# Performance work log

Measured on AMD Instinct MI355X. Metric: run time of the kernel, lower is better.

Reference implementation:

```python
import jax, jax.numpy as jnp
import numpy as np

WIN = (2, 6, 12)          # (vert, lat, lon) window size
HEADS = 6
DIM = 192
TYPES = 64                # type_of_windows = ceil(8/2)*ceil(96/6)
N = WIN[0] * WIN[1] * WIN[2]   # 144 patches per window


def _position_index():
    wz, wh, ww = WIN
    zi = np.arange(wz); zj = -np.arange(wz) * wz
    hi = np.arange(wh); hj = -np.arange(wh) * wh
    w = np.arange(ww)
    c1 = np.stack(np.meshgrid(zi, hi, w, indexing='ij')).reshape(3, -1)
    c2 = np.stack(np.meshgrid(zj, hj, w, indexing='ij')).reshape(3, -1)
    coords = (c1[:, :, None] - c2[:, None, :]).transpose(1, 2, 0)  # (N, N, 3)
    coords[:, :, 2] += ww - 1
    coords[:, :, 1] *= 2 * ww - 1
    coords[:, :, 0] *= (2 * ww - 1) * wh * wh
    return coords.sum(-1).reshape(-1)  # (N*N,) int

POS_IDX = jnp.asarray(_position_index())


def setup_inputs() -> dict:
    key = jax.random.key(0)
    ks = jax.random.split(key, 7)
    B = 960   # n_batch(1) * type_of_windows(64) * lon_windows(15)
    return {
        "x": jax.random.normal(ks[0], (B, N, DIM), jnp.float32),
        "mask": jax.random.normal(ks[1], (15, N, N), jnp.float32),
        "w_qkv": jax.random.normal(ks[2], (DIM, 3 * DIM), jnp.float32) * 0.02,
        "b_qkv": jax.random.normal(ks[3], (3 * DIM,), jnp.float32) * 0.02,
        "w_out": jax.random.normal(ks[4], (DIM, DIM), jnp.float32) * 0.02,
        "b_out": jax.random.normal(ks[5], (DIM,), jnp.float32) * 0.02,
        "bias_table": jax.random.normal(ks[6], (3312, TYPES, HEADS), jnp.float32) * 0.02,
    }


def reference(x, mask, w_qkv, b_qkv, w_out, b_out, bias_table):
    B = x.shape[0]
    hd = DIM // HEADS
    scale = hd ** -0.5

    qkv = (x @ w_qkv + b_qkv).reshape(B, N, 3, HEADS, hd)
    q, k, v = jnp.transpose(qkv, (2, 0, 3, 1, 4))      # each (B, H, N, hd)

    attn = jnp.einsum('bhnd,bhmd->bhnm', q * scale, k)  # (B, H, N, N)

    # gathered earth-specific absolute position bias: (TYPES, H, N, N)
    bias = bias_table[POS_IDX].reshape(N, N, TYPES, HEADS).transpose(2, 3, 0, 1)
    attn = (attn.reshape(-1, TYPES, HEADS, N, N) + bias[None]).reshape(B, HEADS, N, N)

    # additive mask over longitude-shifted windows
    n_w = mask.shape[0]
    attn = attn.reshape(B // n_w, n_w, HEADS, N, N) + mask[None, :, None]
    attn = attn.reshape(B, HEADS, N, N)

    attn = jax.nn.softmax(attn, axis=-1)               # dropout = identity (eval)

    out = jnp.einsum('bhnm,bhmd->bhnd', attn, v)       # (B, H, N, hd)
    out = out.transpose(0, 2, 1, 3).reshape(B, N, DIM)
    return out @ w_out + b_out
```

## Files before the change

### kernel.cpp

```cpp
#include <hip/hip_runtime.h>
#include <stdint.h>

typedef __bf16 bf16;
typedef __bf16 bf16x4 __attribute__((ext_vector_type(4)));
typedef __bf16 bf16x8 __attribute__((ext_vector_type(8)));
typedef float  f32x4  __attribute__((ext_vector_type(4)));

#define MFMA16(A, B, C) __builtin_amdgcn_mfma_f32_16x16x32_bf16((A), (B), (C), 0, 0, 0)

#define LOG2E 1.4426950408889634f


__global__ __launch_bounds__(256) void k_prep(const float* __restrict__ wqkv,
                                              const float* __restrict__ wout,
                                              bf16* __restrict__ wqkvt,
                                              bf16* __restrict__ woutt) {
    int i = blockIdx.x * 256 + threadIdx.x;
    if (i < 576 * 192) {
        int blk = i >> 9;
        int within = i & 511;
        int lane = within >> 3, j = within & 7;
        int strip = blk / 6, ks = blk - strip * 6;
        int col = strip * 16 + (lane & 15);
        int k = ks * 32 + (lane >> 4) * 8 + j;
        wqkvt[i] = (bf16)wqkv[k * 576 + col];
    } else {
        int jj = i - 576 * 192;
        int blk = jj >> 9;
        int within = jj & 511;
        int lane = within >> 3, j = within & 7;
        int strip = blk / 6, ks = blk - strip * 6;
        int col = strip * 16 + (lane & 15);
        int k = ks * 32 + (lane >> 4) * 8 + j;
        woutt[jj] = (bf16)wout[k * 192 + col];
    }
}

__global__ __launch_bounds__(256) void k_bias(const float* __restrict__ btab,
                                              bf16* __restrict__ bias) {
    __shared__ float tb[3312];
    const int th = blockIdx.x;
    for (int i = threadIdx.x; i < 3312; i += 256)
        tb[i] = btab[(size_t)i * 384 + th] * LOG2E;
    __syncthreads();
    bf16* op = bias + (size_t)th * 20736;
    for (int o = threadIdx.x; o < 20736; o += 256) {
        int nt = o / 2304, r1 = o - nt * 2304;
        int ct = r1 / 256,  r2 = r1 - ct * 256;
        int l15 = r2 >> 4,  gr = r2 & 15;
        int n = nt * 16 + l15, m = ct * 16 + gr;
        int zn = n / 72, rn = n - zn * 72, hn = rn / 12, wn = rn - hn * 12;
        int zm = m / 72, rm = m - zm * 72, hm = rm / 12, wm = rm - hm * 12;
        int idx = 828 * (zn + 2 * zm) + 23 * (hn + 6 * hm) + (wn - wm + 11);
        op[o] = (bf16)tb[idx];
    }
}

__global__ __launch_bounds__(256) void k_mswz(const float* __restrict__ mask,
                                              float* __restrict__ msw) {
    const int wm = blockIdx.x / 9;
    const int nt = blockIdx.x - wm * 9;
    const int tid = threadIdx.x;
    const int l15 = tid >> 4, gr = tid & 15;
    const float* src = mask + (size_t)wm * 20736 + (size_t)(nt * 16 + l15) * 144 + gr;
    float* dst = msw + (size_t)wm * 20736 + nt * 2304 + tid;
    #pragma unroll
    for (int ct = 0; ct < 9; ++ct)
        dst[ct * 256] = src[ct * 16];
}

__global__ __launch_bounds__(768, 3) void k_qkv(const float* __restrict__ x,
                                                const float* __restrict__ bqkv,
                                                const bf16* __restrict__ wtf,
                                                bf16* __restrict__ qb,
                                                bf16* __restrict__ kb,
                                                bf16* __restrict__ vtb) {
    __shared__ bf16 xs[96][200];
    const int tid = threadIdx.x;
    const int lane = tid & 63;
    const int w = tid >> 6;
    const int l15 = lane & 15;
    const int g = lane >> 4;
    const int c0 = w * 48;
    const int rowbase = blockIdx.x * 96;

    int hs[3], d0s[3], cgs[3];
    float scl[3];
    f32x4 bv[3];
    #pragma unroll
    for (int s = 0; s < 3; ++s) {
        int cbase = c0 + s * 16;
        int cg = cbase / 192;
        int rem = cbase - cg * 192;
        cgs[s] = cg;
        scl[s] = (cg == 0) ? 0.17677669529663687f * LOG2E : 1.0f;
        hs[s] = rem >> 5;
        d0s[s] = (rem & 31) + g * 4;
        bv[s] = *reinterpret_cast<const f32x4*>(bqkv + cbase + g * 4);
    }

    #pragma unroll
    for (int it = 0; it < 6; ++it) {
        int idx = tid + it * 768;
        int r = idx / 48, cp = idx - r * 48;
        f32x4 xa = *reinterpret_cast<const f32x4*>(x + (size_t)(rowbase + r) * 192 + cp * 4);
        bf16x4 v;
        v[0] = (bf16)xa[0]; v[1] = (bf16)xa[1]; v[2] = (bf16)xa[2]; v[3] = (bf16)xa[3];
        *reinterpret_cast<bf16x4*>(&xs[r][cp * 4]) = v;
    }
    __syncthreads();

    for (int half = 0; half < 2; ++half) {
        const int rbase = half * 48;
        f32x4 acc[3][3];
        #pragma unroll
        for (int t = 0; t < 3; ++t)
            #pragma unroll
            for (int s = 0; s < 3; ++s)
                acc[t][s] = (f32x4){0.f, 0.f, 0.f, 0.f};

        #pragma unroll
        for (int ks = 0; ks < 6; ++ks) {
            bf16x8 bfr0 = *reinterpret_cast<const bf16x8*>(&xs[rbase + 0  + l15][ks * 32 + g * 8]);
            bf16x8 bfr1 = *reinterpret_cast<const bf16x8*>(&xs[rbase + 16 + l15][ks * 32 + g * 8]);
            bf16x8 bfr2 = *reinterpret_cast<const bf16x8*>(&xs[rbase + 32 + l15][ks * 32 + g * 8]);
            #pragma unroll
            for (int s = 0; s < 3; ++s) {
                bf16x8 aw = *reinterpret_cast<const bf16x8*>(wtf + (size_t)(((w * 3 + s) * 6 + ks) * 512 + lane * 8));
                acc[0][s] = MFMA16(aw, bfr0, acc[0][s]);
                acc[1][s] = MFMA16(aw, bfr1, acc[1][s]);
                acc[2][s] = MFMA16(aw, bfr2, acc[2][s]);
            }
        }

        #pragma unroll
        for (int t = 0; t < 3; ++t) {
            const int row0 = rowbase + rbase + t * 16;
            const int bidx = row0 / 144;
            const int n = row0 - bidx * 144 + l15;
            #pragma unroll
            for (int s = 0; s < 3; ++s) {
                float v0 = (acc[t][s][0] + bv[s][0]) * scl[s];
                float v1 = (acc[t][s][1] + bv[s][1]) * scl[s];
                float v2 = (acc[t][s][2] + bv[s][2]) * scl[s];
                float v3 = (acc[t][s][3] + bv[s][3]) * scl[s];
                if (cgs[s] == 2) {
                    bf16* dst = vtb + ((size_t)(bidx * 6 + hs[s]) * 32 + d0s[s]) * 144 + n;
                    dst[0]   = (bf16)v0;
                    dst[144] = (bf16)v1;
                    dst[288] = (bf16)v2;
                    dst[432] = (bf16)v3;
                } else {
                    bf16x4 sv;
                    sv[0] = (bf16)v0; sv[1] = (bf16)v1; sv[2] = (bf16)v2; sv[3] = (bf16)v3;
                    bf16* base = (cgs[s] == 0) ? qb : kb;
                    *reinterpret_cast<bf16x4*>(base + ((size_t)(bidx * 6 + hs[s]) * 144 + n) * 32 + d0s[s]) = sv;
                }
            }
        }
    }
}

__global__ __launch_bounds__(192, 3) void k_attn(const bf16* __restrict__ qb,
                                                 const bf16* __restrict__ kb,
                                                 const bf16* __restrict__ vtb,
                                                 const float* __restrict__ msw,
                                                 const bf16* __restrict__ bias,
                                                 bf16* __restrict__ ob) {
    __shared__ bf16 pl[48][168];
    const int hb = blockIdx.x;
    const int b = hb / 6;
    const int h = hb - b * 6;
    const int t = b & 63;
    const int wm = b % 15;
    const int tid = threadIdx.x;
    const int lane = tid & 63;
    const int wv = tid >> 6;
    const int l15 = lane & 15;
    const int g = lane >> 4;

    const bf16* qp = qb + (size_t)hb * 4608;
    const bf16* kp = kb + (size_t)hb * 4608;
    const bf16* vp = vtb + (size_t)hb * 4608;

    bf16x8 kf[9];
    #pragma unroll
    for (int ct = 0; ct < 9; ++ct)
        kf[ct] = *reinterpret_cast<const bf16x8*>(kp + (size_t)(ct * 16 + l15) * 32 + g * 8);
    bf16x8 vf[10];
    #pragma unroll
    for (int mc = 0; mc < 5; ++mc) {
        vf[mc]     = *reinterpret_cast<const bf16x8*>(vp + (size_t)l15 * 144 + mc * 32 + g * 8);
        vf[5 + mc] = *reinterpret_cast<const bf16x8*>(vp + (size_t)(16 + l15) * 144 + mc * 32 + g * 8);
    }

    if (lane < 32) {
        bf16x8 z;
        #pragma unroll
        for (int i = 0; i < 8; ++i) z[i] = (bf16)0.f;
        *reinterpret_cast<bf16x8*>(&pl[wv * 16 + (lane >> 1)][144 + (lane & 1) * 8]) = z;
    }

    const float* mbase = msw + (size_t)wm * 20736 + l15 * 16 + g * 4;
    const bf16* bbase = bias + (size_t)(t * 6 + h) * 20736 + l15 * 16 + g * 4;

    for (int j = 0; j < 3; ++j) {
        const int n = j * 48 + wv * 16 + l15;
        const int nt = j * 3 + wv;

        bf16x8 bq = *reinterpret_cast<const bf16x8*>(qp + (size_t)n * 32 + g * 8);
        f32x4 s[9];
        #pragma unroll
        for (int ct = 0; ct < 9; ++ct) {
            f32x4 z = (f32x4){0.f, 0.f, 0.f, 0.f};
            s[ct] = MFMA16(kf[ct], bq, z);
        }

        const bf16* brow = bbase + nt * 2304;
        const float* mrow = mbase + nt * 2304;
        #pragma unroll
        for (int ct = 0; ct < 9; ++ct) {
            bf16x4 bvv = *reinterpret_cast<const bf16x4*>(brow + ct * 256);
            f32x4 mv = *reinterpret_cast<const f32x4*>(mrow + ct * 256);
            #pragma unroll
            for (int r = 0; r < 4; ++r)
                s[ct][r] = exp2f(fmaf(mv[r], LOG2E, s[ct][r] + (float)bvv[r]));
        }

        f32x4 sm4 = s[8];
        #pragma unroll
        for (int ct = 0; ct < 4; ++ct) {
            #pragma unroll
            for (int r = 0; r < 4; ++r)
                sm4[r] += s[ct][r] + s[ct + 4][r];
        }
        float rsum = (sm4[0] + sm4[1]) + (sm4[2] + sm4[3]);
        rsum += __shfl_xor(rsum, 16);
        rsum += __shfl_xor(rsum, 32);
        const float rinv = 1.0f / rsum;

        #pragma unroll
        for (int ct = 0; ct < 9; ++ct) {
            bf16x4 pv;
            #pragma unroll
            for (int r = 0; r < 4; ++r) pv[r] = (bf16)s[ct][r];
            *reinterpret_cast<bf16x4*>(&pl[wv * 16 + l15][ct * 16 + g * 4]) = pv;
        }
        __asm__ __volatile__("s_waitcnt lgkmcnt(0)" ::: "memory");

        f32x4 o0 = (f32x4){0.f, 0.f, 0.f, 0.f};
        f32x4 o1 = (f32x4){0.f, 0.f, 0.f, 0.f};
        #pragma unroll
        for (int mc = 0; mc < 5; ++mc) {
            bf16x8 pa = *reinterpret_cast<const bf16x8*>(&pl[wv * 16 + l15][mc * 32 + g * 8]);
            o0 = MFMA16(vf[mc], pa, o0);
            o1 = MFMA16(vf[5 + mc], pa, o1);
        }
        bf16* op = ob + (size_t)b * 27648 + (size_t)n * 192 + h * 32;
        bf16x4 s0, s1;
        #pragma unroll
        for (int r = 0; r < 4; ++r) { s0[r] = (bf16)(o0[r] * rinv); s1[r] = (bf16)(o1[r] * rinv); }
        *reinterpret_cast<bf16x4*>(op + g * 4)      = s0;
        *reinterpret_cast<bf16x4*>(op + 16 + g * 4) = s1;
    }
}

__global__ __launch_bounds__(768, 3) void k_out(const bf16* __restrict__ ob,
                                                const bf16* __restrict__ wtf,
                                                const float* __restrict__ bout,
                                                float* __restrict__ out) {
    __shared__ bf16 os[96][200];
    const int tid = threadIdx.x;
    const int lane = tid & 63;
    const int w = tid >> 6;
    const int l15 = lane & 15;
    const int g = lane >> 4;
    const int c0 = w * 16;
    const int rowbase = blockIdx.x * 96;

    f32x4 bv = *reinterpret_cast<const f32x4*>(bout + c0 + g * 4);

    #pragma unroll
    for (int it = 0; it < 3; ++it) {
        int idx = tid + it * 768;
        int r = idx / 24, cp = idx - r * 24;
        bf16x8 v = *reinterpret_cast<const bf16x8*>(ob + (size_t)(rowbase + r) * 192 + cp * 8);
        *reinterpret_cast<bf16x8*>(&os[r][cp * 8]) = v;
    }
    __syncthreads();

    for (int half = 0; half < 2; ++half) {
        const int rbase = half * 48;
        f32x4 acc[3];
        #pragma unroll
        for (int t = 0; t < 3; ++t) acc[t] = (f32x4){0.f, 0.f, 0.f, 0.f};
        #pragma unroll
        for (int ks = 0; ks < 6; ++ks) {
            bf16x8 bfr0 = *reinterpret_cast<const bf16x8*>(&os[rbase + 0  + l15][ks * 32 + g * 8]);
            bf16x8 bfr1 = *reinterpret_cast<const bf16x8*>(&os[rbase + 16 + l15][ks * 32 + g * 8]);
            bf16x8 bfr2 = *reinterpret_cast<const bf16x8*>(&os[rbase + 32 + l15][ks * 32 + g * 8]);
            bf16x8 aw = *reinterpret_cast<const bf16x8*>(wtf + (size_t)((w * 6 + ks) * 512 + lane * 8));
            acc[0] = MFMA16(aw, bfr0, acc[0]);
            acc[1] = MFMA16(aw, bfr1, acc[1]);
            acc[2] = MFMA16(aw, bfr2, acc[2]);
        }
        #pragma unroll
        for (int t = 0; t < 3; ++t) {
            const int nn = rowbase + rbase + t * 16 + l15;
            f32x4 v;
            v[0] = acc[t][0] + bv[0];
            v[1] = acc[t][1] + bv[1];
            v[2] = acc[t][2] + bv[2];
            v[3] = acc[t][3] + bv[3];
            *reinterpret_cast<f32x4*>(out + (size_t)nn * 192 + c0 + g * 4) = v;
        }
    }
}

extern "C" void kernel_launch(void* const* d_in, const int* in_sizes, int n_in,
                              void* d_out, int out_size, void* d_ws, size_t ws_size,
                              hipStream_t stream) {
    const float* x    = (const float*)d_in[0];
    const float* mask = (const float*)d_in[1];
    const float* wqkv = (const float*)d_in[2];
    const float* bqkv = (const float*)d_in[3];
    const float* wout = (const float*)d_in[4];
    const float* bout = (const float*)d_in[5];
    const float* btab = (const float*)d_in[6];
    float* out = (float*)d_out;

    char* ws = (char*)d_ws;
    bf16* wqkvt = (bf16*)(ws);
    bf16* woutt = (bf16*)(ws + 221184);
    bf16* bias  = (bf16*)(ws + 294912);
    bf16* obuf  = (bf16*)(ws + 16220160);
    bf16* qb    = (bf16*)(ws + 69304320);
    bf16* kb    = (bf16*)(ws + 122388480);
    bf16* vtb   = (bf16*)(ws + 175472640);
    float* msw  = (float*)(ws + 228556800);

    hipLaunchKernelGGL(k_prep, dim3(576),  dim3(256), 0, stream, wqkv, wout, wqkvt, woutt);
    hipLaunchKernelGGL(k_bias, dim3(384),  dim3(256), 0, stream, btab, bias);
    hipLaunchKernelGGL(k_mswz, dim3(135),  dim3(256), 0, stream, mask, msw);
    hipLaunchKernelGGL(k_qkv,  dim3(1440), dim3(768), 0, stream, x, bqkv, wqkvt, qb, kb, vtb);
    hipLaunchKernelGGL(k_attn, dim3(5760), dim3(192), 0, stream, qb, kb, vtb, msw, bias, obuf);
    hipLaunchKernelGGL(k_out,  dim3(1440), dim3(768), 0, stream, obuf, woutt, bout, out);
}
```

Measured before the change: 241.1 us.

## Switch QKV and output projections to 32x32x16 MFMA tiles

Reworks the weight pre-layout and both projection GEMM kernels to use 32x32x16 bf16 MFMA instead of 16x16x32. Each wave now covers 64 output columns (QKV) or 32 columns (out) across all 96 rows in one pass, replacing the two-half loop. Block sizes shrink to 576 and 384 threads. The goal is fewer redundant LDS reads of x per MFMA and better per-instruction throughput. In exchange, each wave holds more accumulator registers and there are fewer waves per block, which may lower occupancy.

```diff
diff --git a/kernel.cpp b/kernel.cpp
--- a/kernel.cpp
+++ b/kernel.cpp
@@ -5,8 +5,10 @@
 typedef __bf16 bf16x4 __attribute__((ext_vector_type(4)));
 typedef __bf16 bf16x8 __attribute__((ext_vector_type(8)));
 typedef float  f32x4  __attribute__((ext_vector_type(4)));
+typedef float  f32x16 __attribute__((ext_vector_type(16)));
 
 #define MFMA16(A, B, C) __builtin_amdgcn_mfma_f32_16x16x32_bf16((A), (B), (C), 0, 0, 0)
+#define MFMA32(A, B, C) __builtin_amdgcn_mfma_f32_32x32x16_bf16((A), (B), (C), 0, 0, 0)
 
 #define LOG2E 1.4426950408889634f
 
@@ -20,18 +22,18 @@
         int blk = i >> 9;
         int within = i & 511;
         int lane = within >> 3, j = within & 7;
-        int strip = blk / 6, ks = blk - strip * 6;
-        int col = strip * 16 + (lane & 15);
-        int k = ks * 32 + (lane >> 4) * 8 + j;
+        int ct = blk / 12, ks = blk - ct * 12;
+        int col = ct * 32 + (lane & 31);
+        int k = ks * 16 + (lane >> 5) * 8 + j;
         wqkvt[i] = (bf16)wqkv[k * 576 + col];
     } else {
         int jj = i - 576 * 192;
         int blk = jj >> 9;
         int within = jj & 511;
         int lane = within >> 3, j = within & 7;
-        int strip = blk / 6, ks = blk - strip * 6;
-        int col = strip * 16 + (lane & 15);
-        int k = ks * 32 + (lane >> 4) * 8 + j;
+        int ct = blk / 12, ks = blk - ct * 12;
+        int col = ct * 32 + (lane & 31);
+        int k = ks * 16 + (lane >> 5) * 8 + j;
         woutt[jj] = (bf16)wout[k * 192 + col];
     }
 }
@@ -69,7 +71,7 @@
         dst[ct * 256] = src[ct * 16];
 }
 
-__global__ __launch_bounds__(768, 3) void k_qkv(const float* __restrict__ x,
+__global__ __launch_bounds__(576, 2) void k_qkv(const float* __restrict__ x,
                                                 const float* __restrict__ bqkv,
                                                 const bf16* __restrict__ wtf,
                                                 bf16* __restrict__ qb,
@@ -79,29 +81,16 @@
     const int tid = threadIdx.x;
     const int lane = tid & 63;
     const int w = tid >> 6;
-    const int l15 = lane & 15;
-    const int g = lane >> 4;
-    const int c0 = w * 48;
+    const int l31 = lane & 31;
+    const int hi = lane >> 5;
+    const int cg = w / 3;
+    const int cwave = w * 64;
     const int rowbase = blockIdx.x * 96;
-
-    int hs[3], d0s[3], cgs[3];
-    float scl[3];
-    f32x4 bv[3];
-    #pragma unroll
-    for (int s = 0; s < 3; ++s) {
-        int cbase = c0 + s * 16;
-        int cg = cbase / 192;
-        int rem = cbase - cg * 192;
-        cgs[s] = cg;
-        scl[s] = (cg == 0) ? 0.17677669529663687f * LOG2E : 1.0f;
-        hs[s] = rem >> 5;
-        d0s[s] = (rem & 31) + g * 4;
-        bv[s] = *reinterpret_cast<const f32x4*>(bqkv + cbase + g * 4);
-    }
-
-    #pragma unroll
-    for (int it = 0; it < 6; ++it) {
-        int idx = tid + it * 768;
+    const float scl = (cg == 0) ? 0.17677669529663687f * LOG2E : 1.0f;
+
+    #pragma unroll
+    for (int it = 0; it < 8; ++it) {
+        int idx = tid + it * 576;
         int r = idx / 48, cp = idx - r * 48;
         f32x4 xa = *reinterpret_cast<const f32x4*>(x + (size_t)(rowbase + r) * 192 + cp * 4);
         bf16x4 v;
@@ -110,51 +99,52 @@
     }
     __syncthreads();
 
-    for (int half = 0; half < 2; ++half) {
-        const int rbase = half * 48;
-        f32x4 acc[3][3];
-        #pragma unroll
-        for (int t = 0; t < 3; ++t)
+    f32x16 a00{}, a01{}, a10{}, a11{}, a20{}, a21{};
+    const size_t wbase0 = (size_t)((w * 2 + 0) * 12) * 512 + lane * 8;
+    const size_t wbase1 = (size_t)((w * 2 + 1) * 12) * 512 + lane * 8;
+    #pragma unroll
+    for (int ks = 0; ks < 12; ++ks) {
+        bf16x8 aw0 = *reinterpret_cast<const bf16x8*>(wtf + wbase0 + ks * 512);
+        bf16x8 aw1 = *reinterpret_cast<const bf16x8*>(wtf + wbase1 + ks * 512);
+        bf16x8 b0 = *reinterpret_cast<const bf16x8*>(&xs[0  + l31][ks * 16 + hi * 8]);
+        bf16x8 b1 = *reinterpret_cast<const bf16x8*>(&xs[32 + l31][ks * 16 + hi * 8]);
+        bf16x8 b2 = *reinterpret_cast<const bf16x8*>(&xs[64 + l31][ks * 16 + hi * 8]);
+        a00 = MFMA32(aw0, b0, a00);  a01 = MFMA32(aw1, b0, a01);
+        a10 = MFMA32(aw0, b1, a10);  a11 = MFMA32(aw1, b1, a11);
+        a20 = MFMA32(aw0, b2, a20);  a21 = MFMA32(aw1, b2, a21);
+    }
+
+    const int rem = cwave - cg * 192;
+    bf16* qkbase = (cg == 0) ? qb : kb;
+    #pragma unroll
+    for (int rt = 0; rt < 3; ++rt) {
+        const unsigned ng = rowbase + rt * 32 + l31;
+        const int bidx = ng / 144;
+        const int n = ng - bidx * 144;
+        #pragma unroll
+        for (int ct2 = 0; ct2 < 2; ++ct2) {
+            const f32x16 av = (rt == 0) ? (ct2 ? a01 : a00)
+                            : (rt == 1) ? (ct2 ? a11 : a10)
+                                        : (ct2 ? a21 : a20);
+            const int h = (rem + ct2 * 32) >> 5;
             #pragma unroll
-            for (int s = 0; s < 3; ++s)
-                acc[t][s] = (f32x4){0.f, 0.f, 0.f, 0.f};
-
-        #pragma unroll
-        for (int ks = 0; ks < 6; ++ks) {
-            bf16x8 bfr0 = *reinterpret_cast<const bf16x8*>(&xs[rbase + 0  + l15][ks * 32 + g * 8]);
-            bf16x8 bfr1 = *reinterpret_cast<const bf16x8*>(&xs[rbase + 16 + l15][ks * 32 + g * 8]);
-            bf16x8 bfr2 = *reinterpret_cast<const bf16x8*>(&xs[rbase + 32 + l15][ks * 32 + g * 8]);
-            #pragma unroll
-            for (int s = 0; s < 3; ++s) {
-                bf16x8 aw = *reinterpret_cast<const bf16x8*>(wtf + (size_t)(((w * 3 + s) * 6 + ks) * 512 + lane * 8));
-                acc[0][s] = MFMA16(aw, bfr0, acc[0][s]);
-                acc[1][s] = MFMA16(aw, bfr1, acc[1][s]);
-                acc[2][s] = MFMA16(aw, bfr2, acc[2][s]);
-            }
-        }
-
-        #pragma unroll
-        for (int t = 0; t < 3; ++t) {
-            const int row0 = rowbase + rbase + t * 16;
-            const int bidx = row0 / 144;
-            const int n = row0 - bidx * 144 + l15;
-            #pragma unroll
-            for (int s = 0; s < 3; ++s) {
-                float v0 = (acc[t][s][0] + bv[s][0]) * scl[s];
-                float v1 = (acc[t][s][1] + bv[s][1]) * scl[s];
-                float v2 = (acc[t][s][2] + bv[s][2]) * scl[s];
-                float v3 = (acc[t][s][3] + bv[s][3]) * scl[s];
-                if (cgs[s] == 2) {
-                    bf16* dst = vtb + ((size_t)(bidx * 6 + hs[s]) * 32 + d0s[s]) * 144 + n;
-                    dst[0]   = (bf16)v0;
-                    dst[144] = (bf16)v1;
-                    dst[288] = (bf16)v2;
-                    dst[432] = (bf16)v3;
+            for (int rg = 0; rg < 4; ++rg) {
+                const int d0 = rg * 8 + hi * 4;
+                f32x4 bvv = *reinterpret_cast<const f32x4*>(bqkv + cwave + ct2 * 32 + d0);
+                float v0 = (av[rg * 4 + 0] + bvv[0]) * scl;
+                float v1 = (av[rg * 4 + 1] + bvv[1]) * scl;
+                float v2 = (av[rg * 4 + 2] + bvv[2]) * scl;
+                float v3 = (av[rg * 4 + 3] + bvv[3]) * scl;
+                if (cg == 2) {
+                    bf16* dst = vtb + ((size_t)(bidx * 6 + h) * 32 + d0) * 144 + n;
+                    dst[0]       = (bf16)v0;
+                    dst[144]     = (bf16)v1;
+                    dst[288]     = (bf16)v2;
+                    dst[432]     = (bf16)v3;
                 } else {
                     bf16x4 sv;
                     sv[0] = (bf16)v0; sv[1] = (bf16)v1; sv[2] = (bf16)v2; sv[3] = (bf16)v3;
-                    bf16* base = (cgs[s] == 0) ? qb : kb;
-                    *reinterpret_cast<bf16x4*>(base + ((size_t)(bidx * 6 + hs[s]) * 144 + n) * 32 + d0s[s]) = sv;
+                    *reinterpret_cast<bf16x4*>(qkbase + ((size_t)(bidx * 6 + h) * 144 + n) * 32 + d0) = sv;
                 }
             }
         }
@@ -265,7 +255,7 @@
     }
 }
 
-__global__ __launch_bounds__(768, 3) void k_out(const bf16* __restrict__ ob,
+__global__ __launch_bounds__(384, 2) void k_out(const bf16* __restrict__ ob,
                                                 const bf16* __restrict__ wtf,
                                                 const float* __restrict__ bout,
                                                 float* __restrict__ out) {
@@ -273,46 +263,47 @@
     const int tid = threadIdx.x;
     const int lane = tid & 63;
     const int w = tid >> 6;
-    const int l15 = lane & 15;
-    const int g = lane >> 4;
-    const int c0 = w * 16;
+    const int l31 = lane & 31;
+    const int hi = lane >> 5;
+    const int cbase = w * 32;
     const int rowbase = blockIdx.x * 96;
 
-    f32x4 bv = *reinterpret_cast<const f32x4*>(bout + c0 + g * 4);
-
-    #pragma unroll
-    for (int it = 0; it < 3; ++it) {
-        int idx = tid + it * 768;
+    #pragma unroll
+    for (int it = 0; it < 6; ++it) {
+        int idx = tid + it * 384;
         int r = idx / 24, cp = idx - r * 24;
         bf16x8 v = *reinterpret_cast<const bf16x8*>(ob + (size_t)(rowbase + r) * 192 + cp * 8);
         *reinterpret_cast<bf16x8*>(&os[r][cp * 8]) = v;
     }
     __syncthreads();
 
-    for (int half = 0; half < 2; ++half) {
-        const int rbase = half * 48;
-        f32x4 acc[3];
-        #pragma unroll
-        for (int t = 0; t < 3; ++t) acc[t] = (f32x4){0.f, 0.f, 0.f, 0.f};
-        #pragma unroll
-        for (int ks = 0; ks < 6; ++ks) {
-            bf16x8 bfr0 = *reinterpret_cast<const bf16x8*>(&os[rbase + 0  + l15][ks * 32 + g * 8]);
-            bf16x8 bfr1 = *reinterpret_cast<const bf16x8*>(&os[rbase + 16 + l15][ks * 32 + g * 8]);
-            bf16x8 bfr2 = *reinterpret_cast<const bf16x8*>(&os[rbase + 32 + l15][ks * 32 + g * 8]);
-            bf16x8 aw = *reinterpret_cast<const bf16x8*>(wtf + (size_t)((w * 6 + ks) * 512 + lane * 8));
-            acc[0] = MFMA16(aw, bfr0, acc[0]);
-            acc[1] = MFMA16(aw, bfr1, acc[1]);
-            acc[2] = MFMA16(aw, bfr2, acc[2]);
-        }
-        #pragma unroll
-        for (int t = 0; t < 3; ++t) {
-            const int nn = rowbase + rbase + t * 16 + l15;
+    f32x16 a0{}, a1{}, a2{};
+    const size_t wbase = (size_t)(w * 12) * 512 + lane * 8;
+    #pragma unroll
+    for (int ks = 0; ks < 12; ++ks) {
+        bf16x8 aw = *reinterpret_cast<const bf16x8*>(wtf + wbase + ks * 512);
+        bf16x8 b0 = *reinterpret_cast<const bf16x8*>(&os[0  + l31][ks * 16 + hi * 8]);
+        bf16x8 b1 = *reinterpret_cast<const bf16x8*>(&os[32 + l31][ks * 16 + hi * 8]);
+        bf16x8 b2 = *reinterpret_cast<const bf16x8*>(&os[64 + l31][ks * 16 + hi * 8]);
+        a0 = MFMA32(aw, b0, a0);
+        a1 = MFMA32(aw, b1, a1);
+        a2 = MFMA32(aw, b2, a2);
+    }
+
+    #pragma unroll
+    for (int rt = 0; rt < 3; ++rt) {
+        const f32x16 av = (rt == 0) ? a0 : (rt == 1) ? a1 : a2;
+        const int n = rowbase + rt * 32 + l31;
+        #pragma unroll
+        for (int rg = 0; rg < 4; ++rg) {
+            const int c4 = cbase + rg * 8 + hi * 4;
+            f32x4 bvv = *reinterpret_cast<const f32x4*>(bout + c4);
             f32x4 v;
-            v[0] = acc[t][0] + bv[0];
-            v[1] = acc[t][1] + bv[1];
-            v[2] = acc[t][2] + bv[2];
-            v[3] = acc[t][3] + bv[3];
-            *reinterpret_cast<f32x4*>(out + (size_t)nn * 192 + c0 + g * 4) = v;
+            v[0] = av[rg * 4 + 0] + bvv[0];
+            v[1] = av[rg * 4 + 1] + bvv[1];
+            v[2] = av[rg * 4 + 2] + bvv[2];
+            v[3] = av[rg * 4 + 3] + bvv[3];
+            *reinterpret_cast<f32x4*>(out + (size_t)n * 192 + c4) = v;
         }
     }
 }
@@ -342,7 +333,7 @@
     hipLaunchKernelGGL(k_prep, dim3(576),  dim3(256), 0, stream, wqkv, wout, wqkvt, woutt);
     hipLaunchKernelGGL(k_bias, dim3(384),  dim3(256), 0, stream, btab, bias);
     hipLaunchKernelGGL(k_mswz, dim3(135),  dim3(256), 0, stream, mask, msw);
-    hipLaunchKernelGGL(k_qkv,  dim3(1440), dim3(768), 0, stream, x, bqkv, wqkvt, qb, kb, vtb);
+    hipLaunchKernelGGL(k_qkv,  dim3(1440), dim3(576), 0, stream, x, bqkv, wqkvt, qb, kb, vtb);
     hipLaunchKernelGGL(k_attn, dim3(5760), dim3(192), 0, stream, qb, kb, vtb, msw, bias, obuf);
-    hipLaunchKernelGGL(k_out,  dim3(1440), dim3(768), 0, stream, obuf, woutt, bout, out);
-}
+    hipLaunchKernelGGL(k_out,  dim3(1440), dim3(384), 0, stream, obuf, woutt, bout, out);
+}
```

Result: slower. 264.7 us (+9.8%).
